# Kernel optimization log

Hardware: AMD Instinct MI355X
Metric: run time of the kernel (lower is better)

Reference implementation:

```python
import jax, jax.numpy as jnp
import numpy as np

NUM_HEADS = 32
HEAD_DIM = 32  # hard-coded in the module


def _rope_sincos(seq_len, head_dim):
    # NOTE: module uses arange(0, head_dim)/head_dim (full dim, not the usual /2 stride)
    inv_freq = 1.0 / (10000.0 ** (jnp.arange(0, head_dim, dtype=jnp.float32) / head_dim))
    freqs = jnp.outer(jnp.arange(seq_len, dtype=jnp.float32), inv_freq)  # [S, D]
    # original repeats over heads then reshapes -> identical values per head,
    # so broadcasting with shape [1, S, 1, D] is equivalent.
    return jnp.sin(freqs)[None, :, None, :], jnp.cos(freqs)[None, :, None, :]


def _apply_rope(x, sin, cos):
    x1, x2 = jnp.split(x, 2, axis=-1)
    x_rot = jnp.concatenate([-x2, x1], axis=-1)
    return x * cos + x_rot * sin


def setup_inputs() -> dict:
    key = jax.random.key(0)
    B, S, H, D = 2, 2048, NUM_HEADS, HEAD_DIM
    dm = H * D
    k1, k2 = jax.random.split(key)
    x = jax.random.normal(k1, (B, S, dm), dtype=jnp.float32)
    W_qkv = jax.random.normal(k2, (dm, 3 * dm), dtype=jnp.float32) / np.sqrt(dm).astype(np.float32)
    mask = jnp.tril(jnp.ones((S, S), dtype=bool))[None, None]  # causal, [1,1,S,S]
    return {"x": x, "W_qkv": W_qkv, "mask": mask}


def reference(x, W_qkv, mask):
    B, S, dm = x.shape
    H, D = NUM_HEADS, HEAD_DIM
    qkv = x @ W_qkv  # [B, S, 3*H*D], no bias
    q, k, v = jnp.split(qkv, 3, axis=-1)
    q = q.reshape(B, S, H, D)
    k = k.reshape(B, S, H, D)
    v = v.reshape(B, S, H, D)

    sin, cos = _rope_sincos(S, D)
    q = _apply_rope(q, sin, cos)
    k = _apply_rope(k, sin, cos)

    # [B, H, S, D]
    q = q.transpose(0, 2, 1, 3)
    k = k.transpose(0, 2, 1, 3)
    v = v.transpose(0, 2, 1, 3)

    scale = 1.0 / np.sqrt(D).astype(np.float32)
    attn = jnp.einsum('bhqd,bhkd->bhqk', q, k) * scale  # [B, H, S, S]
    attn = jnp.where(mask, attn, jnp.float32(-jnp.inf))
    attn = jax.nn.softmax(attn, axis=-1)
    out = jnp.einsum('bhqk,bhkd->bhqd', attn, v)  # [B, H, S, D]
    return out.transpose(0, 2, 1, 3).reshape(B, S, H * D)
```

## Files before the change

kernel.cpp:

```cpp
#include <hip/hip_runtime.h>
#include <cstdint>
#include <cstddef>

#define BB 2
#define SS 2048
#define HH 32
#define DD 32
#define DM 1024
#define MROWS 4096
#define NQKV 3072

#define QSCALE 0.25503486f

typedef __attribute__((ext_vector_type(8))) short bf16x8;
typedef __attribute__((ext_vector_type(4))) float f32x4;
typedef __attribute__((address_space(1))) unsigned int gu32;
typedef __attribute__((address_space(3))) unsigned int lu32;

__device__ __forceinline__ unsigned short f2bf(float f) {
    union { float f; unsigned int u; } v;
    v.f = f;
    unsigned int u = v.u;
    u += 0x7fffu + ((u >> 16) & 1u);
    return (unsigned short)(u >> 16);
}

__device__ __forceinline__ unsigned int cvt_pk_bf16(float a, float b) {
    unsigned int r;
    asm("v_cvt_pk_bf16_f32 %0, %1, %2" : "=v"(r) : "v"(a), "v"(b));
    return r;
}
__device__ __forceinline__ unsigned short bf1(float a) {
    return (unsigned short)cvt_pk_bf16(a, a);
}

__global__ __launch_bounds__(256) void prep_k(
        const float* __restrict__ x, const float* __restrict__ w,
        unsigned short* __restrict__ xb, unsigned short* __restrict__ wT,
        float* __restrict__ tk, float* __restrict__ tq) {
    __shared__ unsigned short tile[64][65];
    const int blk = blockIdx.x;
    const int tid = threadIdx.x;
    if (blk < 4096) {
        const int i = blk * 256 + tid;
        float4 v = ((const float4*)x)[i];
        ushort4 o;
        o.x = f2bf(v.x); o.y = f2bf(v.y); o.z = f2bf(v.z); o.w = f2bf(v.w);
        ((ushort4*)xb)[i] = o;
    } else if (blk < 4864) {
        const int bx = blk - 4096;
        const int n0 = (bx % 48) * 64;
        const int k0 = (bx / 48) * 64;
        const int tx = tid & 63;
        const int ty = tid >> 6;
        for (int i = ty; i < 64; i += 4)
            tile[i][tx] = f2bf(w[(size_t)(k0 + i) * NQKV + n0 + tx]);
        __syncthreads();
        for (int i = ty; i < 64; i += 4)
            wT[(size_t)(n0 + i) * 1024 + k0 + tx] = tile[tx][i];
    } else {
        const int i = (blk - 4864) * 256 + tid;
        const int s = i >> 4, dl = i & 15;
        const float inv1 = exp2f((float)dl * -0.41524101186092029f);
        const float inv2 = exp2f((float)(dl + 16) * -0.41524101186092029f);
        float s1, c1, s2, c2;
        sincosf((float)s * inv1, &s1, &c1);
        sincosf((float)s * inv2, &s2, &c2);
        float4 vk = {s1, c1, s2, c2};
        float4 vq = {s1 * QSCALE, c1 * QSCALE, s2 * QSCALE, c2 * QSCALE};
        ((float4*)tk)[i] = vk;
        ((float4*)tq)[i] = vq;
    }
}

__global__ __launch_bounds__(256) void qkv_gemm_k(
        const unsigned short* __restrict__ xb,
        const unsigned short* __restrict__ wTp,
        const float4* __restrict__ tk, const float4* __restrict__ tq,
        unsigned short* __restrict__ qbuf,
        unsigned short* __restrict__ kbuf,
        unsigned short* __restrict__ vtbuf) {
    __shared__ unsigned short smem[2 * 8192];
    const int m0 = blockIdx.x * 128;
    const int n0 = blockIdx.y * 128;
    const int tid = threadIdx.x;
    const int w = tid >> 6, lane = tid & 63;
    const int quad = lane >> 4, l16 = lane & 15;
    const int wr = w >> 1, wc = w & 1;

    f32x4 acc[4][4];
#pragma unroll
    for (int i = 0; i < 4; ++i)
#pragma unroll
        for (int j = 0; j < 4; ++j)
            acc[i][j] = (f32x4){0.f, 0.f, 0.f, 0.f};

    const int G = (lane & 56) | ((lane ^ (lane >> 3)) & 7);
    const int goff = (G >> 2) * 1024 + (G & 3) * 8;
    const int Gr = l16 * 4 + quad;
    const int L = Gr ^ ((Gr >> 3) & 7);
    const int roff = L * 8;

#define QKV_STAGE(k0, buf)                                                          \
    do {                                                                            \
        unsigned short* As_ = smem + (buf) * 8192;                                  \
        unsigned short* Bs_ = As_ + 4096;                                           \
        _Pragma("unroll")                                                           \
        for (int q = 0; q < 2; ++q) {                                               \
            const int seg = w * 2 + q;                                              \
            const unsigned short* ga = xb  + (size_t)(m0 + seg * 16) * 1024 + (k0) + goff; \
            const unsigned short* gb = wTp + (size_t)(n0 + seg * 16) * 1024 + (k0) + goff; \
            __builtin_amdgcn_global_load_lds((gu32*)ga, (lu32*)(As_ + seg * 512), 16, 0, 0); \
            __builtin_amdgcn_global_load_lds((gu32*)gb, (lu32*)(Bs_ + seg * 512), 16, 0, 0); \
        }                                                                           \
    } while (0)

    QKV_STAGE(0, 0);
    __syncthreads();
    int cur = 0;
    for (int kt = 0; kt < 32; ++kt) {
        if (kt < 31) QKV_STAGE((kt + 1) * 32, cur ^ 1);
        const unsigned short* As = smem + cur * 8192;
        const unsigned short* Bs = As + 4096;
        bf16x8 af[4], bfv[4];
#pragma unroll
        for (int i = 0; i < 4; ++i)
            af[i] = *(const bf16x8*)(As + (wr * 4 + i) * 512 + roff);
#pragma unroll
        for (int j = 0; j < 4; ++j)
            bfv[j] = *(const bf16x8*)(Bs + (wc * 4 + j) * 512 + roff);
#pragma unroll
        for (int i = 0; i < 4; ++i)
#pragma unroll
            for (int j = 0; j < 4; ++j)
                acc[i][j] = __builtin_amdgcn_mfma_f32_16x16x32_bf16(af[i], bfv[j], acc[i][j], 0, 0, 0);
        __syncthreads();
        cur ^= 1;
    }
#undef QKV_STAGE

    const int sec = n0 >> 10;
    const int rowb = m0 + wr * 64;
    const int colb = n0 + wc * 64;
    if (sec < 2) {
        unsigned short* dst = (sec == 0) ? qbuf : kbuf;
        const float4* tab = (sec == 0) ? tq : tk;
        const int h0 = (colb & 1023) >> 5;
        const int h1 = ((colb + 32) & 1023) >> 5;
#pragma unroll
        for (int i = 0; i < 4; ++i) {
#pragma unroll
            for (int r = 0; r < 4; ++r) {
                const int row = rowb + i * 16 + quad * 4 + r;
                const int bb = row >> 11, s = row & 2047;
                const float4 t = tab[s * 16 + l16];
                unsigned short* pb = dst + ((size_t)(bb * 32) * 2048 + s) * 32;
                {
                    const float x1 = acc[i][0][r], x2 = acc[i][1][r];
                    unsigned short* p = pb + (size_t)h0 * (2048 * 32);
                    p[l16]      = bf1(x1 * t.y - x2 * t.x);
                    p[l16 + 16] = bf1(x2 * t.w + x1 * t.z);
                }
                {
                    const float x1 = acc[i][2][r], x2 = acc[i][3][r];
                    unsigned short* p = pb + (size_t)h1 * (2048 * 32);
                    p[l16]      = bf1(x1 * t.y - x2 * t.x);
                    p[l16 + 16] = bf1(x2 * t.w + x1 * t.z);
                }
            }
        }
    } else {
        __syncthreads();
        unsigned short* tw = smem + w * 2048;
        const int bbi = rowb >> 11;
        const int srow = rowb & 2047;
        const int colB = colb - 2048;
#pragma unroll
        for (int j = 0; j < 4; ++j) {
#pragma unroll
            for (int i = 0; i < 4; ++i) {
                uint2 pk;
                pk.x = cvt_pk_bf16(acc[i][j][0], acc[i][j][1]);
                pk.y = cvt_pk_bf16(acc[i][j][2], acc[i][j][3]);
                *(uint2*)&tw[l16 * 66 + i * 16 + quad * 4] = pk;
            }
#pragma unroll
            for (int c = 0; c < 16; ++c) {
                const int col = colB + j * 16 + c;
                const int hh = col >> 5, d = col & 31;
                vtbuf[((size_t)(bbi * 32 + hh) * 32 + d) * 2048 + srow + lane] = tw[c * 66 + lane];
            }
        }
    }
}

#define ATTN_TILE(KC0, KC1, VC0, VC1, KP0, KP1, VP0, VP1, A00, A01, A10, A11, LS0, LS1, PLW) \
    {                                                                                \
        KP0 += 2048; KP1 += 2048; VP0 += 64; VP1 += 64;                              \
        bf16x8 kn0 = *(const bf16x8*)KP0;                                            \
        bf16x8 kn1 = *(const bf16x8*)KP1;                                            \
        bf16x8 vn0 = *(const bf16x8*)VP0;                                            \
        bf16x8 vn1 = *(const bf16x8*)VP1;                                            \
        f32x4 s00 = __builtin_amdgcn_mfma_f32_16x16x32_bf16(KC0, qf0, fz, 0, 0, 0);  \
        f32x4 s01 = __builtin_amdgcn_mfma_f32_16x16x32_bf16(KC0, qf1, fz, 0, 0, 0);  \
        f32x4 s10 = __builtin_amdgcn_mfma_f32_16x16x32_bf16(KC1, qf0, fz, 0, 0, 0);  \
        f32x4 s11 = __builtin_amdgcn_mfma_f32_16x16x32_bf16(KC1, qf1, fz, 0, 0, 0);  \
        unsigned short (*plw)[40] = PLW;                                             \
        {                                                                            \
            float p0 = __builtin_amdgcn_exp2f(s00[0]), p1 = __builtin_amdgcn_exp2f(s00[1]); \
            float p2 = __builtin_amdgcn_exp2f(s00[2]), p3 = __builtin_amdgcn_exp2f(s00[3]); \
            LS0 += (p0 + p1) + (p2 + p3);                                            \
            uint2 pk; pk.x = cvt_pk_bf16(p0, p1); pk.y = cvt_pk_bf16(p2, p3);        \
            *(uint2*)&plw[l16][quad * 4] = pk;                                       \
        }                                                                            \
        {                                                                            \
            float p0 = __builtin_amdgcn_exp2f(s01[0]), p1 = __builtin_amdgcn_exp2f(s01[1]); \
            float p2 = __builtin_amdgcn_exp2f(s01[2]), p3 = __builtin_amdgcn_exp2f(s01[3]); \
            LS1 += (p0 + p1) + (p2 + p3);                                            \
            uint2 pk; pk.x = cvt_pk_bf16(p0, p1); pk.y = cvt_pk_bf16(p2, p3);        \
            *(uint2*)&plw[16 + l16][quad * 4] = pk;                                  \
        }                                                                            \
        {                                                                            \
            float p0 = __builtin_amdgcn_exp2f(s10[0]), p1 = __builtin_amdgcn_exp2f(s10[1]); \
            float p2 = __builtin_amdgcn_exp2f(s10[2]), p3 = __builtin_amdgcn_exp2f(s10[3]); \
            LS0 += (p0 + p1) + (p2 + p3);                                            \
            uint2 pk; pk.x = cvt_pk_bf16(p0, p1); pk.y = cvt_pk_bf16(p2, p3);        \
            *(uint2*)&plw[l16][16 + quad * 4] = pk;                                  \
        }                                                                            \
        {                                                                            \
            float p0 = __builtin_amdgcn_exp2f(s11[0]), p1 = __builtin_amdgcn_exp2f(s11[1]); \
            float p2 = __builtin_amdgcn_exp2f(s11[2]), p3 = __builtin_amdgcn_exp2f(s11[3]); \
            LS1 += (p0 + p1) + (p2 + p3);                                            \
            uint2 pk; pk.x = cvt_pk_bf16(p0, p1); pk.y = cvt_pk_bf16(p2, p3);        \
            *(uint2*)&plw[16 + l16][16 + quad * 4] = pk;                             \
        }                                                                            \
        bf16x8 pf0 = *(const bf16x8*)&plw[l16][quad * 8];                            \
        bf16x8 pf1 = *(const bf16x8*)&plw[16 + l16][quad * 8];                       \
        A00 = __builtin_amdgcn_mfma_f32_16x16x32_bf16(VC0, pf0, A00, 0, 0, 0);       \
        A01 = __builtin_amdgcn_mfma_f32_16x16x32_bf16(VC0, pf1, A01, 0, 0, 0);       \
        A10 = __builtin_amdgcn_mfma_f32_16x16x32_bf16(VC1, pf0, A10, 0, 0, 0);       \
        A11 = __builtin_amdgcn_mfma_f32_16x16x32_bf16(VC1, pf1, A11, 0, 0, 0);       \
        KC0 = kn0; KC1 = kn1; VC0 = vn0; VC1 = vn1;                                  \
    }

#define ATTN_DIAG(KC0, KC1, VC0, VC1, A00, A01, A10, A11, LS0, LS1, PLW)             \
    {                                                                                \
        f32x4 s00 = __builtin_amdgcn_mfma_f32_16x16x32_bf16(KC0, qf0, fz, 0, 0, 0);  \
        f32x4 s01 = __builtin_amdgcn_mfma_f32_16x16x32_bf16(KC0, qf1, fz, 0, 0, 0);  \
        f32x4 s11 = __builtin_amdgcn_mfma_f32_16x16x32_bf16(KC1, qf1, fz, 0, 0, 0);  \
        unsigned short (*plw)[40] = PLW;                                             \
        {                                                                            \
            float p[4];                                                              \
            _Pragma("unroll")                                                        \
            for (int r = 0; r < 4; ++r)                                              \
                p[r] = (quad * 4 + r > l16) ? 0.f : __builtin_amdgcn_exp2f(s00[r]);  \
            LS0 += (p[0] + p[1]) + (p[2] + p[3]);                                    \
            uint2 pk; pk.x = cvt_pk_bf16(p[0], p[1]); pk.y = cvt_pk_bf16(p[2], p[3]); \
            *(uint2*)&plw[l16][quad * 4] = pk;                                       \
        }                                                                            \
        {                                                                            \
            float p0 = __builtin_amdgcn_exp2f(s01[0]), p1 = __builtin_amdgcn_exp2f(s01[1]); \
            float p2 = __builtin_amdgcn_exp2f(s01[2]), p3 = __builtin_amdgcn_exp2f(s01[3]); \
            LS1 += (p0 + p1) + (p2 + p3);                                            \
            uint2 pk; pk.x = cvt_pk_bf16(p0, p1); pk.y = cvt_pk_bf16(p2, p3);        \
            *(uint2*)&plw[16 + l16][quad * 4] = pk;                                  \
        }                                                                            \
        {                                                                            \
            uint2 pk; pk.x = 0; pk.y = 0;                                            \
            *(uint2*)&plw[l16][16 + quad * 4] = pk;                                  \
        }                                                                            \
        {                                                                            \
            float p[4];                                                              \
            _Pragma("unroll")                                                        \
            for (int r = 0; r < 4; ++r)                                              \
                p[r] = (quad * 4 + r > l16) ? 0.f : __builtin_amdgcn_exp2f(s11[r]);  \
            LS1 += (p[0] + p[1]) + (p[2] + p[3]);                                    \
            uint2 pk; pk.x = cvt_pk_bf16(p[0], p[1]); pk.y = cvt_pk_bf16(p[2], p[3]); \
            *(uint2*)&plw[16 + l16][16 + quad * 4] = pk;                             \
        }                                                                            \
        bf16x8 pf0 = *(const bf16x8*)&plw[l16][quad * 8];                            \
        bf16x8 pf1 = *(const bf16x8*)&plw[16 + l16][quad * 8];                       \
        A00 = __builtin_amdgcn_mfma_f32_16x16x32_bf16(VC0, pf0, A00, 0, 0, 0);       \
        A01 = __builtin_amdgcn_mfma_f32_16x16x32_bf16(VC0, pf1, A01, 0, 0, 0);       \
        A10 = __builtin_amdgcn_mfma_f32_16x16x32_bf16(VC1, pf0, A10, 0, 0, 0);       \
        A11 = __builtin_amdgcn_mfma_f32_16x16x32_bf16(VC1, pf1, A11, 0, 0, 0);       \
    }

__global__ __launch_bounds__(256) void attn_k(
        const unsigned short* __restrict__ qb,
        const unsigned short* __restrict__ kb,
        const unsigned short* __restrict__ vt,
        float* __restrict__ out) {
    __shared__ unsigned short Pl[4][2][2][32][40];
    const int tid = threadIdx.x;
    const int w = tid >> 6, lane = tid & 63;
    const int quad = lane >> 4, l16 = lane & 15;
    const int i = blockIdx.x;
    const int xcd = i & 7;
    const int slot = i >> 3;
    const int bh = ((slot & 7) << 3) | xcd;
    const int pr = slot >> 3;
    const int b = bh >> 5, h = bh & 31;

    const unsigned short* qbase = qb + (size_t)bh * 2048 * 32;
    const unsigned short* kbase = kb + (size_t)bh * 2048 * 32;
    const unsigned short* vbase = vt + (size_t)bh * 32 * 2048;
    const f32x4 fz = {0.f, 0.f, 0.f, 0.f};

    for (int ph = 0; ph < 2; ++ph) {
        const int qw = (ph == 0) ? (pr * 128 + w * 32)
                                 : ((15 - pr) * 128 + (3 - w) * 32);
        const int nkt = (qw >> 5) + 1;
        const int m = nkt - 1;
        const int mA = (m + 1) >> 1;
        const int mB = m >> 1;

        bf16x8 qf0 = *(const bf16x8*)(qbase + (size_t)(qw + l16) * 32 + quad * 8);
        bf16x8 qf1 = *(const bf16x8*)(qbase + (size_t)(qw + 16 + l16) * 32 + quad * 8);

        f32x4 aA00 = fz, aA01 = fz, aA10 = fz, aA11 = fz;
        float lsA0 = 0.f, lsA1 = 0.f;
        const unsigned short* kpA0 = kbase + (size_t)l16 * 32 + quad * 8;
        const unsigned short* kpA1 = kbase + (size_t)(16 + l16) * 32 + quad * 8;
        const unsigned short* vpA0 = vbase + (size_t)l16 * 2048 + quad * 8;
        const unsigned short* vpA1 = vbase + (size_t)(16 + l16) * 2048 + quad * 8;
        bf16x8 kcA0 = *(const bf16x8*)kpA0;
        bf16x8 kcA1 = *(const bf16x8*)kpA1;
        bf16x8 vcA0 = *(const bf16x8*)vpA0;
        bf16x8 vcA1 = *(const bf16x8*)vpA1;

        f32x4 aB00 = fz, aB01 = fz, aB10 = fz, aB11 = fz;
        float lsB0 = 0.f, lsB1 = 0.f;
        const unsigned short* kpB0 = kpA0 + 1024;
        const unsigned short* kpB1 = kpA1 + 1024;
        const unsigned short* vpB0 = vpA0 + 32;
        const unsigned short* vpB1 = vpA1 + 32;
        bf16x8 kcB0 = *(const bf16x8*)kpB0;
        bf16x8 kcB1 = *(const bf16x8*)kpB1;
        bf16x8 vcB0 = *(const bf16x8*)vpB0;
        bf16x8 vcB1 = *(const bf16x8*)vpB1;

        for (int it = 0; it < mA; ++it) {
            ATTN_TILE(kcA0, kcA1, vcA0, vcA1, kpA0, kpA1, vpA0, vpA1,
                      aA00, aA01, aA10, aA11, lsA0, lsA1, Pl[w][0][it & 1]);
            if (it < mB) {
                ATTN_TILE(kcB0, kcB1, vcB0, vcB1, kpB0, kpB1, vpB0, vpB1,
                          aB00, aB01, aB10, aB11, lsB0, lsB1, Pl[w][1][it & 1]);
            }
        }

        if (m & 1) {
            ATTN_DIAG(kcB0, kcB1, vcB0, vcB1, aB00, aB01, aB10, aB11,
                      lsB0, lsB1, Pl[w][1][mB & 1]);
        } else {
            ATTN_DIAG(kcA0, kcA1, vcA0, vcA1, aA00, aA01, aA10, aA11,
                      lsA0, lsA1, Pl[w][0][mA & 1]);
        }

        f32x4 a00 = aA00 + aB00, a01 = aA01 + aB01;
        f32x4 a10 = aA10 + aB10, a11 = aA11 + aB11;
        float ls0 = lsA0 + lsB0, ls1 = lsA1 + lsB1;

        float l0 = ls0; l0 += __shfl_xor(l0, 16); l0 += __shfl_xor(l0, 32);
        float l1 = ls1; l1 += __shfl_xor(l1, 16); l1 += __shfl_xor(l1, 32);
        const float inv0 = 1.f / l0, inv1 = 1.f / l1;

        float* ot = (float*)&Pl[w][0][0][0][0];
        {
            f32x4 t;
            t = a00; t[0]*=inv0; t[1]*=inv0; t[2]*=inv0; t[3]*=inv0;
            *(f32x4*)&ot[(l16) * 36 + quad * 4] = t;
            t = a10; t[0]*=inv0; t[1]*=inv0; t[2]*=inv0; t[3]*=inv0;
            *(f32x4*)&ot[(l16) * 36 + 16 + quad * 4] = t;
            t = a01; t[0]*=inv1; t[1]*=inv1; t[2]*=inv1; t[3]*=inv1;
            *(f32x4*)&ot[(16 + l16) * 36 + quad * 4] = t;
            t = a11; t[0]*=inv1; t[1]*=inv1; t[2]*=inv1; t[3]*=inv1;
            *(f32x4*)&ot[(16 + l16) * 36 + 16 + quad * 4] = t;
        }
        const int dd = lane & 31, qpar = lane >> 5;
        float* ob = out + (size_t)(b * 2048 + qw) * 1024 + h * 32;
#pragma unroll
        for (int i2 = 0; i2 < 16; ++i2) {
            const int qloc = i2 * 2 + qpar;
            ob[(size_t)qloc * 1024 + dd] = ot[qloc * 36 + dd];
        }
    }
}

extern "C" void kernel_launch(void* const* d_in, const int* in_sizes, int n_in,
                              void* d_out, int out_size, void* d_ws, size_t ws_size,
                              hipStream_t stream) {
    (void)in_sizes; (void)n_in; (void)out_size; (void)ws_size;
    const float* x = (const float*)d_in[0];
    const float* wq = (const float*)d_in[1];
    float* out = (float*)d_out;

    unsigned short* xb = (unsigned short*)d_ws;
    unsigned short* wT = xb + (size_t)MROWS * DM;
    unsigned short* qb = wT + (size_t)NQKV * DM;
    unsigned short* kb = qb + (size_t)BB * HH * SS * DD;
    unsigned short* vt = kb + (size_t)BB * HH * SS * DD;
    float* tk = (float*)(vt + (size_t)BB * HH * SS * DD);
    float* tq = tk + (size_t)SS * 16 * 4;

    prep_k<<<dim3(4992), dim3(256), 0, stream>>>(x, wq, xb, wT, tk, tq);
    qkv_gemm_k<<<dim3(MROWS / 128, NQKV / 128), dim3(256), 0, stream>>>(
        xb, wT, (const float4*)tk, (const float4*)tq, qb, kb, vt);
    attn_k<<<dim3(BB * HH * 8), dim3(256), 0, stream>>>(qb, kb, vt, out);
}
```

Baseline: 179.1 us.

## Replace dual-chain attention loop with 3-deep rotating K/V register prefetch

Drops the two independent accumulator chains (A/B, each double-buffering its next K/V tile) in favour of a single accumulator set with a three-slot rotating register buffer. Each tile's K and V loads are issued right after their MFMA uses, about three tiles ahead. The loop is unrolled by three with a remainder and a diagonal-tile dispatch, and the LDS P buffers become three slots per wave. The aim is to hide global load latency with deeper prefetch while freeing accumulator registers, at the cost of a serial dependence through the single accumulator set and less independent MFMA work per iteration.

```diff
diff --git a/kernel.cpp b/kernel.cpp
--- a/kernel.cpp
+++ b/kernel.cpp
@@ -194,56 +194,55 @@
     }
 }
 
-#define ATTN_TILE(KC0, KC1, VC0, VC1, KP0, KP1, VP0, VP1, A00, A01, A10, A11, LS0, LS1, PLW) \
+#define ATTN_TILE(KC0, KC1, VC0, VC1, PLW)                                           \
     {                                                                                \
-        KP0 += 2048; KP1 += 2048; VP0 += 64; VP1 += 64;                              \
-        bf16x8 kn0 = *(const bf16x8*)KP0;                                            \
-        bf16x8 kn1 = *(const bf16x8*)KP1;                                            \
-        bf16x8 vn0 = *(const bf16x8*)VP0;                                            \
-        bf16x8 vn1 = *(const bf16x8*)VP1;                                            \
         f32x4 s00 = __builtin_amdgcn_mfma_f32_16x16x32_bf16(KC0, qf0, fz, 0, 0, 0);  \
         f32x4 s01 = __builtin_amdgcn_mfma_f32_16x16x32_bf16(KC0, qf1, fz, 0, 0, 0);  \
         f32x4 s10 = __builtin_amdgcn_mfma_f32_16x16x32_bf16(KC1, qf0, fz, 0, 0, 0);  \
         f32x4 s11 = __builtin_amdgcn_mfma_f32_16x16x32_bf16(KC1, qf1, fz, 0, 0, 0);  \
+        KC0 = *(const bf16x8*)kp0;                                                   \
+        KC1 = *(const bf16x8*)kp1;                                                   \
         unsigned short (*plw)[40] = PLW;                                             \
         {                                                                            \
             float p0 = __builtin_amdgcn_exp2f(s00[0]), p1 = __builtin_amdgcn_exp2f(s00[1]); \
             float p2 = __builtin_amdgcn_exp2f(s00[2]), p3 = __builtin_amdgcn_exp2f(s00[3]); \
-            LS0 += (p0 + p1) + (p2 + p3);                                            \
+            ls0 += (p0 + p1) + (p2 + p3);                                            \
             uint2 pk; pk.x = cvt_pk_bf16(p0, p1); pk.y = cvt_pk_bf16(p2, p3);        \
             *(uint2*)&plw[l16][quad * 4] = pk;                                       \
         }                                                                            \
         {                                                                            \
             float p0 = __builtin_amdgcn_exp2f(s01[0]), p1 = __builtin_amdgcn_exp2f(s01[1]); \
             float p2 = __builtin_amdgcn_exp2f(s01[2]), p3 = __builtin_amdgcn_exp2f(s01[3]); \
-            LS1 += (p0 + p1) + (p2 + p3);                                            \
+            ls1 += (p0 + p1) + (p2 + p3);                                            \
             uint2 pk; pk.x = cvt_pk_bf16(p0, p1); pk.y = cvt_pk_bf16(p2, p3);        \
             *(uint2*)&plw[16 + l16][quad * 4] = pk;                                  \
         }                                                                            \
         {                                                                            \
             float p0 = __builtin_amdgcn_exp2f(s10[0]), p1 = __builtin_amdgcn_exp2f(s10[1]); \
             float p2 = __builtin_amdgcn_exp2f(s10[2]), p3 = __builtin_amdgcn_exp2f(s10[3]); \
-            LS0 += (p0 + p1) + (p2 + p3);                                            \
+            ls0 += (p0 + p1) + (p2 + p3);                                            \
             uint2 pk; pk.x = cvt_pk_bf16(p0, p1); pk.y = cvt_pk_bf16(p2, p3);        \
             *(uint2*)&plw[l16][16 + quad * 4] = pk;                                  \
         }                                                                            \
         {                                                                            \
             float p0 = __builtin_amdgcn_exp2f(s11[0]), p1 = __builtin_amdgcn_exp2f(s11[1]); \
             float p2 = __builtin_amdgcn_exp2f(s11[2]), p3 = __builtin_amdgcn_exp2f(s11[3]); \
-            LS1 += (p0 + p1) + (p2 + p3);                                            \
+            ls1 += (p0 + p1) + (p2 + p3);                                            \
             uint2 pk; pk.x = cvt_pk_bf16(p0, p1); pk.y = cvt_pk_bf16(p2, p3);        \
             *(uint2*)&plw[16 + l16][16 + quad * 4] = pk;                             \
         }                                                                            \
         bf16x8 pf0 = *(const bf16x8*)&plw[l16][quad * 8];                            \
         bf16x8 pf1 = *(const bf16x8*)&plw[16 + l16][quad * 8];                       \
-        A00 = __builtin_amdgcn_mfma_f32_16x16x32_bf16(VC0, pf0, A00, 0, 0, 0);       \
-        A01 = __builtin_amdgcn_mfma_f32_16x16x32_bf16(VC0, pf1, A01, 0, 0, 0);       \
-        A10 = __builtin_amdgcn_mfma_f32_16x16x32_bf16(VC1, pf0, A10, 0, 0, 0);       \
-        A11 = __builtin_amdgcn_mfma_f32_16x16x32_bf16(VC1, pf1, A11, 0, 0, 0);       \
-        KC0 = kn0; KC1 = kn1; VC0 = vn0; VC1 = vn1;                                  \
-    }
-
-#define ATTN_DIAG(KC0, KC1, VC0, VC1, A00, A01, A10, A11, LS0, LS1, PLW)             \
+        a00 = __builtin_amdgcn_mfma_f32_16x16x32_bf16(VC0, pf0, a00, 0, 0, 0);       \
+        a01 = __builtin_amdgcn_mfma_f32_16x16x32_bf16(VC0, pf1, a01, 0, 0, 0);       \
+        a10 = __builtin_amdgcn_mfma_f32_16x16x32_bf16(VC1, pf0, a10, 0, 0, 0);       \
+        a11 = __builtin_amdgcn_mfma_f32_16x16x32_bf16(VC1, pf1, a11, 0, 0, 0);       \
+        VC0 = *(const bf16x8*)vp0;                                                   \
+        VC1 = *(const bf16x8*)vp1;                                                   \
+        kp0 += 1024; kp1 += 1024; vp0 += 32; vp1 += 32;                              \
+    }
+
+#define ATTN_DIAG(KC0, KC1, VC0, VC1, PLW)                                           \
     {                                                                                \
         f32x4 s00 = __builtin_amdgcn_mfma_f32_16x16x32_bf16(KC0, qf0, fz, 0, 0, 0);  \
         f32x4 s01 = __builtin_amdgcn_mfma_f32_16x16x32_bf16(KC0, qf1, fz, 0, 0, 0);  \
@@ -254,14 +253,14 @@
             _Pragma("unroll")                                                        \
             for (int r = 0; r < 4; ++r)                                              \
                 p[r] = (quad * 4 + r > l16) ? 0.f : __builtin_amdgcn_exp2f(s00[r]);  \
-            LS0 += (p[0] + p[1]) + (p[2] + p[3]);                                    \
+            ls0 += (p[0] + p[1]) + (p[2] + p[3]);                                    \
             uint2 pk; pk.x = cvt_pk_bf16(p[0], p[1]); pk.y = cvt_pk_bf16(p[2], p[3]); \
             *(uint2*)&plw[l16][quad * 4] = pk;                                       \
         }                                                                            \
         {                                                                            \
             float p0 = __builtin_amdgcn_exp2f(s01[0]), p1 = __builtin_amdgcn_exp2f(s01[1]); \
             float p2 = __builtin_amdgcn_exp2f(s01[2]), p3 = __builtin_amdgcn_exp2f(s01[3]); \
-            LS1 += (p0 + p1) + (p2 + p3);                                            \
+            ls1 += (p0 + p1) + (p2 + p3);                                            \
             uint2 pk; pk.x = cvt_pk_bf16(p0, p1); pk.y = cvt_pk_bf16(p2, p3);        \
             *(uint2*)&plw[16 + l16][quad * 4] = pk;                                  \
         }                                                                            \
@@ -274,16 +273,16 @@
             _Pragma("unroll")                                                        \
             for (int r = 0; r < 4; ++r)                                              \
                 p[r] = (quad * 4 + r > l16) ? 0.f : __builtin_amdgcn_exp2f(s11[r]);  \
-            LS1 += (p[0] + p[1]) + (p[2] + p[3]);                                    \
+            ls1 += (p[0] + p[1]) + (p[2] + p[3]);                                    \
             uint2 pk; pk.x = cvt_pk_bf16(p[0], p[1]); pk.y = cvt_pk_bf16(p[2], p[3]); \
             *(uint2*)&plw[16 + l16][16 + quad * 4] = pk;                             \
         }                                                                            \
         bf16x8 pf0 = *(const bf16x8*)&plw[l16][quad * 8];                            \
         bf16x8 pf1 = *(const bf16x8*)&plw[16 + l16][quad * 8];                       \
-        A00 = __builtin_amdgcn_mfma_f32_16x16x32_bf16(VC0, pf0, A00, 0, 0, 0);       \
-        A01 = __builtin_amdgcn_mfma_f32_16x16x32_bf16(VC0, pf1, A01, 0, 0, 0);       \
-        A10 = __builtin_amdgcn_mfma_f32_16x16x32_bf16(VC1, pf0, A10, 0, 0, 0);       \
-        A11 = __builtin_amdgcn_mfma_f32_16x16x32_bf16(VC1, pf1, A11, 0, 0, 0);       \
+        a00 = __builtin_amdgcn_mfma_f32_16x16x32_bf16(VC0, pf0, a00, 0, 0, 0);       \
+        a01 = __builtin_amdgcn_mfma_f32_16x16x32_bf16(VC0, pf1, a01, 0, 0, 0);       \
+        a10 = __builtin_amdgcn_mfma_f32_16x16x32_bf16(VC1, pf0, a10, 0, 0, 0);       \
+        a11 = __builtin_amdgcn_mfma_f32_16x16x32_bf16(VC1, pf1, a11, 0, 0, 0);       \
     }
 
 __global__ __launch_bounds__(256) void attn_k(
@@ -291,7 +290,7 @@
         const unsigned short* __restrict__ kb,
         const unsigned short* __restrict__ vt,
         float* __restrict__ out) {
-    __shared__ unsigned short Pl[4][2][2][32][40];
+    __shared__ unsigned short Pl[4][3][32][40];
     const int tid = threadIdx.x;
     const int w = tid >> 6, lane = tid & 63;
     const int quad = lane >> 4, l16 = lane & 15;
@@ -312,70 +311,61 @@
                                  : ((15 - pr) * 128 + (3 - w) * 32);
         const int nkt = (qw >> 5) + 1;
         const int m = nkt - 1;
-        const int mA = (m + 1) >> 1;
-        const int mB = m >> 1;
 
         bf16x8 qf0 = *(const bf16x8*)(qbase + (size_t)(qw + l16) * 32 + quad * 8);
         bf16x8 qf1 = *(const bf16x8*)(qbase + (size_t)(qw + 16 + l16) * 32 + quad * 8);
 
-        f32x4 aA00 = fz, aA01 = fz, aA10 = fz, aA11 = fz;
-        float lsA0 = 0.f, lsA1 = 0.f;
-        const unsigned short* kpA0 = kbase + (size_t)l16 * 32 + quad * 8;
-        const unsigned short* kpA1 = kbase + (size_t)(16 + l16) * 32 + quad * 8;
-        const unsigned short* vpA0 = vbase + (size_t)l16 * 2048 + quad * 8;
-        const unsigned short* vpA1 = vbase + (size_t)(16 + l16) * 2048 + quad * 8;
-        bf16x8 kcA0 = *(const bf16x8*)kpA0;
-        bf16x8 kcA1 = *(const bf16x8*)kpA1;
-        bf16x8 vcA0 = *(const bf16x8*)vpA0;
-        bf16x8 vcA1 = *(const bf16x8*)vpA1;
-
-        f32x4 aB00 = fz, aB01 = fz, aB10 = fz, aB11 = fz;
-        float lsB0 = 0.f, lsB1 = 0.f;
-        const unsigned short* kpB0 = kpA0 + 1024;
-        const unsigned short* kpB1 = kpA1 + 1024;
-        const unsigned short* vpB0 = vpA0 + 32;
-        const unsigned short* vpB1 = vpA1 + 32;
-        bf16x8 kcB0 = *(const bf16x8*)kpB0;
-        bf16x8 kcB1 = *(const bf16x8*)kpB1;
-        bf16x8 vcB0 = *(const bf16x8*)vpB0;
-        bf16x8 vcB1 = *(const bf16x8*)vpB1;
-
-        for (int it = 0; it < mA; ++it) {
-            ATTN_TILE(kcA0, kcA1, vcA0, vcA1, kpA0, kpA1, vpA0, vpA1,
-                      aA00, aA01, aA10, aA11, lsA0, lsA1, Pl[w][0][it & 1]);
-            if (it < mB) {
-                ATTN_TILE(kcB0, kcB1, vcB0, vcB1, kpB0, kpB1, vpB0, vpB1,
-                          aB00, aB01, aB10, aB11, lsB0, lsB1, Pl[w][1][it & 1]);
-            }
-        }
-
-        if (m & 1) {
-            ATTN_DIAG(kcB0, kcB1, vcB0, vcB1, aB00, aB01, aB10, aB11,
-                      lsB0, lsB1, Pl[w][1][mB & 1]);
+        f32x4 a00 = fz, a01 = fz, a10 = fz, a11 = fz;
+        float ls0 = 0.f, ls1 = 0.f;
+
+        const unsigned short* kp0 = kbase + (size_t)l16 * 32 + quad * 8;
+        const unsigned short* kp1 = kbase + (size_t)(16 + l16) * 32 + quad * 8;
+        const unsigned short* vp0 = vbase + (size_t)l16 * 2048 + quad * 8;
+        const unsigned short* vp1 = vbase + (size_t)(16 + l16) * 2048 + quad * 8;
+
+        bf16x8 kA0 = *(const bf16x8*)kp0, kA1 = *(const bf16x8*)kp1;
+        bf16x8 vA0 = *(const bf16x8*)vp0, vA1 = *(const bf16x8*)vp1;
+        kp0 += 1024; kp1 += 1024; vp0 += 32; vp1 += 32;
+        bf16x8 kB0 = *(const bf16x8*)kp0, kB1 = *(const bf16x8*)kp1;
+        bf16x8 vB0 = *(const bf16x8*)vp0, vB1 = *(const bf16x8*)vp1;
+        kp0 += 1024; kp1 += 1024; vp0 += 32; vp1 += 32;
+        bf16x8 kC0 = *(const bf16x8*)kp0, kC1 = *(const bf16x8*)kp1;
+        bf16x8 vC0 = *(const bf16x8*)vp0, vC1 = *(const bf16x8*)vp1;
+        kp0 += 1024; kp1 += 1024; vp0 += 32; vp1 += 32;
+
+        int t = 0;
+        for (; t + 3 <= m; t += 3) {
+            ATTN_TILE(kA0, kA1, vA0, vA1, Pl[w][0]);
+            ATTN_TILE(kB0, kB1, vB0, vB1, Pl[w][1]);
+            ATTN_TILE(kC0, kC1, vC0, vC1, Pl[w][2]);
+        }
+        const int r = m - t;
+        if (r > 0) ATTN_TILE(kA0, kA1, vA0, vA1, Pl[w][0]);
+        if (r > 1) ATTN_TILE(kB0, kB1, vB0, vB1, Pl[w][1]);
+
+        if (r == 0) {
+            ATTN_DIAG(kA0, kA1, vA0, vA1, Pl[w][0]);
+        } else if (r == 1) {
+            ATTN_DIAG(kB0, kB1, vB0, vB1, Pl[w][1]);
         } else {
-            ATTN_DIAG(kcA0, kcA1, vcA0, vcA1, aA00, aA01, aA10, aA11,
-                      lsA0, lsA1, Pl[w][0][mA & 1]);
-        }
-
-        f32x4 a00 = aA00 + aB00, a01 = aA01 + aB01;
-        f32x4 a10 = aA10 + aB10, a11 = aA11 + aB11;
-        float ls0 = lsA0 + lsB0, ls1 = lsA1 + lsB1;
+            ATTN_DIAG(kC0, kC1, vC0, vC1, Pl[w][2]);
+        }
 
         float l0 = ls0; l0 += __shfl_xor(l0, 16); l0 += __shfl_xor(l0, 32);
         float l1 = ls1; l1 += __shfl_xor(l1, 16); l1 += __shfl_xor(l1, 32);
         const float inv0 = 1.f / l0, inv1 = 1.f / l1;
 
-        float* ot = (float*)&Pl[w][0][0][0][0];
+        float* ot = (float*)&Pl[w][0][0][0];
         {
-            f32x4 t;
-            t = a00; t[0]*=inv0; t[1]*=inv0; t[2]*=inv0; t[3]*=inv0;
-            *(f32x4*)&ot[(l16) * 36 + quad * 4] = t;
-            t = a10; t[0]*=inv0; t[1]*=inv0; t[2]*=inv0; t[3]*=inv0;
-            *(f32x4*)&ot[(l16) * 36 + 16 + quad * 4] = t;
-            t = a01; t[0]*=inv1; t[1]*=inv1; t[2]*=inv1; t[3]*=inv1;
-            *(f32x4*)&ot[(16 + l16) * 36 + quad * 4] = t;
-            t = a11; t[0]*=inv1; t[1]*=inv1; t[2]*=inv1; t[3]*=inv1;
-            *(f32x4*)&ot[(16 + l16) * 36 + 16 + quad * 4] = t;
+            f32x4 tt;
+            tt = a00; tt[0]*=inv0; tt[1]*=inv0; tt[2]*=inv0; tt[3]*=inv0;
+            *(f32x4*)&ot[(l16) * 36 + quad * 4] = tt;
+            tt = a10; tt[0]*=inv0; tt[1]*=inv0; tt[2]*=inv0; tt[3]*=inv0;
+            *(f32x4*)&ot[(l16) * 36 + 16 + quad * 4] = tt;
+            tt = a01; tt[0]*=inv1; tt[1]*=inv1; tt[2]*=inv1; tt[3]*=inv1;
+            *(f32x4*)&ot[(16 + l16) * 36 + quad * 4] = tt;
+            tt = a11; tt[0]*=inv1; tt[1]*=inv1; tt[2]*=inv1; tt[3]*=inv1;
+            *(f32x4*)&ot[(16 + l16) * 36 + 16 + quad * 4] = tt;
         }
         const int dd = lane & 31, qpar = lane >> 5;
         float* ob = out + (size_t)(b * 2048 + qw) * 1024 + h * 32;
```

Measured after the change: 177.0 us. No clear change (-1.2%).
